# Kernel tuning notes

Hardware: AMD Instinct MI355X
Metric: run time of the kernel (lower is better)

## Reference

```python
import jax, jax.numpy as jnp
import numpy as np
from jax import lax

EMBED_DIM = 384
NUM_GROUPS = 128
GROUP_SIZE = 64
LN_EPS = 1e-5


def setup_inputs() -> dict:
    key = jax.random.key(0)
    k_pts, k1, k2, k3, k4 = jax.random.split(key, 5)
    B, N = 32, 16384
    points = jax.random.normal(k_pts, (B, N, 3), dtype=jnp.float32)
    # local_mlp: Linear(3,128) -> GELU -> Linear(128, embed_dim)
    w1 = jax.random.normal(k1, (3, 128), dtype=jnp.float32) * (1.0 / np.sqrt(3))
    b1 = jax.random.normal(k2, (128,), dtype=jnp.float32) * 0.01
    w2 = jax.random.normal(k3, (128, EMBED_DIM), dtype=jnp.float32) * (1.0 / np.sqrt(128))
    b2 = jax.random.normal(k4, (EMBED_DIM,), dtype=jnp.float32) * 0.01
    ln_scale = jnp.ones((EMBED_DIM,), dtype=jnp.float32)
    ln_bias = jnp.zeros((EMBED_DIM,), dtype=jnp.float32)
    return {"points": points, "w1": w1, "b1": b1, "w2": w2, "b2": b2,
            "ln_scale": ln_scale, "ln_bias": ln_bias}


def _farthest_point_sample(points, num_samples):
    # points: [B, N, 3]. Deterministic start at index 0 (torch uses randint).
    B, N, _ = points.shape

    def step(carry, _):
        distance, farthest = carry  # [B, N], [B]
        centroid = jnp.take_along_axis(points, farthest[:, None, None], axis=1)  # [B,1,3]
        d = jnp.sum((points - centroid) ** 2, axis=-1)  # [B, N]
        distance = jnp.minimum(distance, d)
        nxt = jnp.argmax(distance, axis=-1).astype(jnp.int32)
        return (distance, nxt), farthest

    init = (jnp.full((B, N), jnp.inf, dtype=points.dtype),
            jnp.zeros((B,), dtype=jnp.int32))
    _, idx = lax.scan(step, init, None, length=num_samples)  # [S, B]
    return idx.T  # [B, S]


def reference(points, w1, b1, w2, b2, ln_scale, ln_bias):
    B, N, _ = points.shape
    centroid_idx = _farthest_point_sample(points, NUM_GROUPS)  # [B, G]
    centroids = jnp.take_along_axis(
        points, centroid_idx[:, :, None].astype(jnp.int32), axis=1)  # [B, G, 3]

    # squared distances (same ordering as torch.cdist for topk); matmul form
    # avoids materializing a [B, G, N, 3] diff tensor.
    c2 = jnp.sum(centroids ** 2, axis=-1)  # [B, G]
    p2 = jnp.sum(points ** 2, axis=-1)     # [B, N]
    dist2 = c2[:, :, None] + p2[:, None, :] - 2.0 * jnp.einsum(
        'bgc,bnc->bgn', centroids, points)  # [B, G, N]

    # k smallest -> top_k of negated distances
    _, neighbor_idx = lax.top_k(-dist2, GROUP_SIZE)  # [B, G, K]

    batch_ix = jnp.arange(B)[:, None, None]
    grouped = points[batch_ix, neighbor_idx]  # [B, G, K, 3]
    local_coords = grouped - centroids[:, :, None, :]  # [B, G, K, 3]

    h = jax.nn.gelu(local_coords @ w1 + b1, approximate=False)  # [B,G,K,128]
    feats = h @ w2 + b2  # [B, G, K, D]
    tokens = jnp.mean(feats, axis=2)  # [B, G, D]

    mu = jnp.mean(tokens, axis=-1, keepdims=True)
    var = jnp.mean((tokens - mu) ** 2, axis=-1, keepdims=True)
    tokens_ln = (tokens - mu) * lax.rsqrt(var + LN_EPS) * ln_scale + ln_bias
    return centroids, tokens_ln
```

## Files before the change

### kernel.cpp

```cpp
#include <hip/hip_runtime.h>
#include <math.h>

#define BB 32
#define NN 16384
#define GG 128
#define KK 64
#define HH 128
#define DD 384
#define LN_EPS 1e-5f
#define NBUCK 2048
#define CANDCAP 1024

__device__ __forceinline__ float sq3(float x, float y, float z) {
    return __fadd_rn(__fadd_rn(__fmul_rn(x, x), __fmul_rn(y, y)), __fmul_rn(z, z));
}

__global__ void prep_kernel(const float* __restrict__ w2, float* __restrict__ w2t) {
    int i = blockIdx.x * 256 + threadIdx.x;
    if (i < HH * DD) {
        int f = i >> 7;
        int k = i & 127;
        w2t[i] = w2[k * DD + f];
    }
}

__global__ __launch_bounds__(512) void fps_kernel(const float* __restrict__ pts,
                                                  float* __restrict__ cent_out,
                                                  float4* __restrict__ cent_pad) {
    const int b = blockIdx.x;
    const int tid = threadIdx.x;
    const float* p = pts + (size_t)b * NN * 3;

    float x[32], y[32], z[32], dist[32];
#pragma unroll
    for (int j = 0; j < 32; j++) {
        int n = j * 512 + tid;
        x[j] = p[n * 3 + 0];
        y[j] = p[n * 3 + 1];
        z[j] = p[n * 3 + 2];
        dist[j] = INFINITY;
    }

    __shared__ float cenx, ceny, cenz;
    __shared__ float wv[8];
    __shared__ int wi[8];

    if (tid == 0) { cenx = p[0]; ceny = p[1]; cenz = p[2]; }
    __syncthreads();

    for (int it = 0; it < GG; it++) {
        float cx = cenx, cy = ceny, cz = cenz;
        if (tid == 0) {
            float* co = cent_out + ((size_t)b * GG + it) * 3;
            co[0] = cx; co[1] = cy; co[2] = cz;
            cent_pad[b * GG + it] = make_float4(cx, cy, cz, sq3(cx, cy, cz));
        }
        float bv0 = -INFINITY, bv1 = -INFINITY, bv2 = -INFINITY, bv3 = -INFINITY;
        int bi0 = 0, bi1 = 0, bi2 = 0, bi3 = 0;
#pragma unroll
        for (int j = 0; j < 32; j++) {
            float dx = __fsub_rn(x[j], cx);
            float dy = __fsub_rn(y[j], cy);
            float dz = __fsub_rn(z[j], cz);
            float d = sq3(dx, dy, dz);
            float dj = fminf(dist[j], d);
            dist[j] = dj;
            int n = j * 512 + tid;
            switch (j & 3) {
                case 0: if (dj > bv0) { bv0 = dj; bi0 = n; } break;
                case 1: if (dj > bv1) { bv1 = dj; bi1 = n; } break;
                case 2: if (dj > bv2) { bv2 = dj; bi2 = n; } break;
                case 3: if (dj > bv3) { bv3 = dj; bi3 = n; } break;
            }
        }
        float fv = bv0; int fi = bi0;
        if (bv1 > fv || (bv1 == fv && bi1 < fi)) { fv = bv1; fi = bi1; }
        if (bv2 > fv || (bv2 == fv && bi2 < fi)) { fv = bv2; fi = bi2; }
        if (bv3 > fv || (bv3 == fv && bi3 < fi)) { fv = bv3; fi = bi3; }
#pragma unroll
        for (int off = 32; off >= 1; off >>= 1) {
            float ov = __shfl_down(fv, off);
            int oi = __shfl_down(fi, off);
            if (ov > fv || (ov == fv && oi < fi)) { fv = ov; fi = oi; }
        }
        int lane = tid & 63, wid = tid >> 6;
        if (lane == 0) { wv[wid] = fv; wi[wid] = fi; }
        __syncthreads();
        if (tid == 0) {
            float gv = wv[0]; int gi = wi[0];
            for (int w = 1; w < 8; w++) {
                if (wv[w] > gv || (wv[w] == gv && wi[w] < gi)) { gv = wv[w]; gi = wi[w]; }
            }
            const float* wp = p + (size_t)gi * 3;
            cenx = wp[0]; ceny = wp[1]; cenz = wp[2];
        }
        __syncthreads();
    }
}

__global__ __launch_bounds__(256) void group_kernel(
    const float* __restrict__ pts, const float4* __restrict__ cent_pad,
    const float* __restrict__ w1, const float* __restrict__ b1,
    const float* __restrict__ w2t, const float* __restrict__ b2,
    const float* __restrict__ lns, const float* __restrict__ lnb,
    float* __restrict__ tok_out) {
    __shared__ __align__(16) unsigned hist[NBUCK];
    __shared__ unsigned long long cand[CANDCAP];
    __shared__ int selIdx[KK];
    __shared__ float4 localPt[KK];
    __shared__ float w1s[3 * HH];
    __shared__ float b1s[HH];
    __shared__ __align__(16) float hbar[HH];
    __shared__ float partial[256];
    __shared__ float red2[8];
    __shared__ float toks[DD];
    __shared__ int waveSum[4];
    __shared__ unsigned long long wmin[4];
    __shared__ unsigned TA_S;
    __shared__ int cntS;
    __shared__ unsigned long long lastS;
    __shared__ float muS, rstdS;

    const int tid = threadIdx.x;
    int bid = blockIdx.x;
    int xcd = bid & 7, sub = bid >> 3;
    int b = xcd * 4 + (sub >> 7);
    int g = sub & 127;

    const float* p = pts + (size_t)b * NN * 3;
    float4 c4 = cent_pad[b * GG + g];

    for (int i = tid; i < 3 * HH; i += 256) w1s[i] = w1[i];
    if (tid < HH) b1s[tid] = b1[tid];
    for (int i = tid; i < NBUCK; i += 256) hist[i] = 0;
    if (tid == 0) cntS = 0;
    __syncthreads();

    unsigned key[64];
#pragma unroll
    for (int i = 0; i < 64; i++) {
        int n = i * 256 + tid;
        float px = p[n * 3], py = p[n * 3 + 1], pz = p[n * 3 + 2];
        float p2 = sq3(px, py, pz);
        float dot = __fadd_rn(__fadd_rn(__fmul_rn(c4.x, px), __fmul_rn(c4.y, py)),
                              __fmul_rn(c4.z, pz));
        float d = __fsub_rn(__fadd_rn(c4.w, p2), __fmul_rn(2.0f, dot));
        unsigned u = __float_as_uint(d);
        u ^= (u & 0x80000000u) ? 0xFFFFFFFFu : 0x80000000u;
        key[i] = u;
        atomicAdd(&hist[u >> 21], 1u);
    }
    __syncthreads();

    {
        uint4 h0 = ((const uint4*)hist)[tid * 2];
        uint4 h1 = ((const uint4*)hist)[tid * 2 + 1];
        int loc[8] = {(int)h0.x, (int)h0.y, (int)h0.z, (int)h0.w,
                      (int)h1.x, (int)h1.y, (int)h1.z, (int)h1.w};
        int s = 0;
#pragma unroll
        for (int j = 0; j < 8; j++) s += loc[j];
        int lane = tid & 63, wid = tid >> 6;
        int v = s;
#pragma unroll
        for (int off = 1; off < 64; off <<= 1) {
            int o = __shfl_up(v, off);
            if (lane >= off) v += o;
        }
        if (lane == 63) waveSum[wid] = v;
        __syncthreads();
        int base = 0;
        for (int w = 0; w < wid; w++) base += waveSum[w];
        int c = base + v - s;
#pragma unroll
        for (int j = 0; j < 8; j++) {
            if (c < KK && c + loc[j] >= KK) TA_S = (unsigned)(tid * 8 + j);
            c += loc[j];
        }
        __syncthreads();
    }
    unsigned TA = TA_S;

#pragma unroll
    for (int i = 0; i < 64; i++) {
        unsigned u = key[i];
        if ((u >> 21) <= TA) {
            int pos = atomicAdd(&cntS, 1);
            if (pos < CANDCAP)
                cand[pos] = ((unsigned long long)u << 32) | (unsigned)(i * 256 + tid);
        }
    }
    __syncthreads();
    int cnt = cntS;

    if (cnt <= CANDCAP) {
        for (int c0 = tid; c0 < cnt; c0 += 256) {
            unsigned long long pr = cand[c0];
            int rank = 0;
            for (int j = 0; j < cnt; j++) rank += (cand[j] < pr);
            if (rank < KK) selIdx[rank] = (int)(unsigned)pr;
        }
        __syncthreads();
    } else {
        if (tid == 0) lastS = 0ull;
        __syncthreads();
        for (int r = 0; r < KK; r++) {
            unsigned long long last = lastS;
            unsigned long long best = 0xFFFFFFFFFFFFFFFFull;
#pragma unroll
            for (int i = 0; i < 64; i++) {
                unsigned long long pr =
                    ((unsigned long long)key[i] << 32) | (unsigned)(i * 256 + tid);
                if ((r == 0 || pr > last) && pr < best) best = pr;
            }
            unsigned blo = (unsigned)best, bhi = (unsigned)(best >> 32);
#pragma unroll
            for (int off = 32; off >= 1; off >>= 1) {
                unsigned olo = __shfl_down(blo, off);
                unsigned ohi = __shfl_down(bhi, off);
                unsigned long long ob = ((unsigned long long)ohi << 32) | olo;
                unsigned long long cur = ((unsigned long long)bhi << 32) | blo;
                if (ob < cur) { blo = olo; bhi = ohi; }
            }
            int lane = tid & 63, wid = tid >> 6;
            if (lane == 0) wmin[wid] = ((unsigned long long)bhi << 32) | blo;
            __syncthreads();
            if (tid == 0) {
                unsigned long long m = wmin[0];
                for (int w = 1; w < 4; w++) if (wmin[w] < m) m = wmin[w];
                selIdx[r] = (int)(unsigned)m;
                lastS = m;
            }
            __syncthreads();
        }
    }

    if (tid < KK) {
        int n = selIdx[tid];
        float px = p[n * 3], py = p[n * 3 + 1], pz = p[n * 3 + 2];
        localPt[tid] = make_float4(px - c4.x, py - c4.y, pz - c4.z, 0.f);
    }
    __syncthreads();
    {
        int f = tid & 127, half = tid >> 7;
        float wa = w1s[f], wb = w1s[HH + f], wc = w1s[2 * HH + f], bb = b1s[f];
        float s = 0.f;
        for (int k = half * 32; k < half * 32 + 32; k++) {
            float4 lp = localPt[k];
            float a = lp.x * wa + lp.y * wb + lp.z * wc + bb;
            float hh = 0.5f * a * (1.0f + erff(a * 0.70710678118654752440f));
            s += hh;
        }
        partial[tid] = s;
    }
    __syncthreads();
    if (tid < HH) hbar[tid] = (partial[tid] + partial[tid + HH]) * (1.0f / 64.0f);
    __syncthreads();
    for (int f2 = tid; f2 < DD; f2 += 256) {
        const float4* wrow = (const float4*)(w2t + f2 * HH);
        const float4* hb = (const float4*)hbar;
        float acc = b2[f2];
#pragma unroll 8
        for (int q = 0; q < 32; q++) {
            float4 w4 = wrow[q];
            float4 h4 = hb[q];
            acc += h4.x * w4.x + h4.y * w4.y + h4.z * w4.z + h4.w * w4.w;
        }
        toks[f2] = acc;
    }
    __syncthreads();
    {
        float s1 = 0.f, s2 = 0.f;
        for (int f2 = tid; f2 < DD; f2 += 256) {
            float v = toks[f2];
            s1 += v;
            s2 += v * v;
        }
#pragma unroll
        for (int off = 32; off >= 1; off >>= 1) {
            s1 += __shfl_down(s1, off);
            s2 += __shfl_down(s2, off);
        }
        int lane = tid & 63, wid = tid >> 6;
        if (lane == 0) { partial[wid] = s1; red2[wid] = s2; }
        __syncthreads();
        if (tid == 0) {
            float t1 = partial[0] + partial[1] + partial[2] + partial[3];
            float t2 = red2[0] + red2[1] + red2[2] + red2[3];
            float mu = t1 / (float)DD;
            float var = t2 / (float)DD - mu * mu;
            muS = mu;
            rstdS = rsqrtf(var + LN_EPS);
        }
        __syncthreads();
    }
    float mu = muS, rstd = rstdS;
    float* outp = tok_out + ((size_t)b * GG + g) * DD;
    for (int f2 = tid; f2 < DD; f2 += 256) {
        outp[f2] = (toks[f2] - mu) * rstd * lns[f2] + lnb[f2];
    }
}

extern "C" void kernel_launch(void* const* d_in, const int* in_sizes, int n_in,
                              void* d_out, int out_size, void* d_ws, size_t ws_size,
                              hipStream_t stream) {
    const float* pts = (const float*)d_in[0];
    const float* w1 = (const float*)d_in[1];
    const float* b1 = (const float*)d_in[2];
    const float* w2 = (const float*)d_in[3];
    const float* b2 = (const float*)d_in[4];
    const float* lns = (const float*)d_in[5];
    const float* lnb = (const float*)d_in[6];
    float* out = (float*)d_out;

    float4* cent_pad = (float4*)d_ws;
    float* w2t = (float*)((char*)d_ws + BB * GG * sizeof(float4));

    prep_kernel<<<192, 256, 0, stream>>>(w2, w2t);
    fps_kernel<<<BB, 512, 0, stream>>>(pts, out, cent_pad);
    group_kernel<<<BB * GG, 256, 0, stream>>>(pts, cent_pad, w1, b1, w2t, b2, lns, lnb,
                                              out + BB * GG * 3);
}
```

Baseline: 629.9 us.

## Split FPS across four blocks per batch and use wave-per-group kNN selection

```diff
diff --git a/kernel.cpp b/kernel.cpp
--- a/kernel.cpp
+++ b/kernel.cpp
@@ -8,296 +8,299 @@
 #define HH 128
 #define DD 384
 #define LN_EPS 1e-5f
-#define NBUCK 2048
-#define CANDCAP 1024
+#define CAP 1024
+#define FPSB 4
+#define FPSP (NN / FPSB)
 
 __device__ __forceinline__ float sq3(float x, float y, float z) {
     return __fadd_rn(__fadd_rn(__fmul_rn(x, x), __fmul_rn(y, y)), __fmul_rn(z, z));
 }
 
-__global__ void prep_kernel(const float* __restrict__ w2, float* __restrict__ w2t) {
+__device__ __forceinline__ unsigned distkey(float px, float py, float pz, float4 c4) {
+    float p2 = sq3(px, py, pz);
+    float dot = __fadd_rn(__fadd_rn(__fmul_rn(c4.x, px), __fmul_rn(c4.y, py)),
+                          __fmul_rn(c4.z, pz));
+    float d = __fsub_rn(__fadd_rn(c4.w, p2), __fmul_rn(2.0f, dot));
+    unsigned u = __float_as_uint(d);
+    return u ^ ((u & 0x80000000u) ? 0xFFFFFFFFu : 0x80000000u);
+}
+
+__device__ __forceinline__ unsigned lanerank(unsigned long long m) {
+    unsigned r = __builtin_amdgcn_mbcnt_lo((unsigned)m, 0);
+    return __builtin_amdgcn_mbcnt_hi((unsigned)(m >> 32), r);
+}
+
+__global__ void prep_kernel(const float* __restrict__ w2, float* __restrict__ w2t,
+                            unsigned* __restrict__ zeroArea) {
     int i = blockIdx.x * 256 + threadIdx.x;
     if (i < HH * DD) {
-        int f = i >> 7;
-        int k = i & 127;
+        int f = i >> 7, k = i & 127;
         w2t[i] = w2[k * DD + f];
     }
-}
-
-__global__ __launch_bounds__(512) void fps_kernel(const float* __restrict__ pts,
-                                                  float* __restrict__ cent_out,
-                                                  float4* __restrict__ cent_pad) {
-    const int b = blockIdx.x;
-    const int tid = threadIdx.x;
-    const float* p = pts + (size_t)b * NN * 3;
-
-    float x[32], y[32], z[32], dist[32];
-#pragma unroll
-    for (int j = 0; j < 32; j++) {
-        int n = j * 512 + tid;
-        x[j] = p[n * 3 + 0];
-        y[j] = p[n * 3 + 1];
-        z[j] = p[n * 3 + 2];
-        dist[j] = INFINITY;
-    }
-
-    __shared__ float cenx, ceny, cenz;
+    int j = i - HH * DD;
+    if (j >= 0 && j < 12288) zeroArea[j] = 0u;
+}
+
+__global__ __launch_bounds__(512, 2) void fps_kernel(
+    const float* __restrict__ pts, float* __restrict__ cent_out,
+    float4* __restrict__ cent_pad, unsigned long long* __restrict__ gslot,
+    unsigned* __restrict__ garr) {
+    __shared__ float xs[FPSP], ys[FPSP], zs[FPSP], ds[FPSP];
     __shared__ float wv[8];
     __shared__ int wi[8];
-
-    if (tid == 0) { cenx = p[0]; ceny = p[1]; cenz = p[2]; }
+    __shared__ float cen[2][3];
+    const int tid = threadIdx.x;
+    const int x = blockIdx.x & 7, j = blockIdx.x >> 3;
+    const int b = x * 4 + (j >> 2), quarter = j & 3;
+    const float* pb = pts + (size_t)b * NN * 3;
+    const int start = quarter * FPSP;
+    const float4* p4s = (const float4*)(pb + start * 3);
+
+    for (int t = tid; t < FPSP / 4; t += 512) {
+        float4 A = p4s[3 * t], Bv = p4s[3 * t + 1], Cv = p4s[3 * t + 2];
+        ((float4*)xs)[t] = make_float4(A.x, A.w, Bv.z, Cv.y);
+        ((float4*)ys)[t] = make_float4(A.y, Bv.x, Bv.w, Cv.z);
+        ((float4*)zs)[t] = make_float4(A.z, Bv.y, Cv.x, Cv.w);
+        ((float4*)ds)[t] = make_float4(INFINITY, INFINITY, INFINITY, INFINITY);
+    }
     __syncthreads();
 
+    float cx = pb[0], cy = pb[1], cz = pb[2];
+
     for (int it = 0; it < GG; it++) {
-        float cx = cenx, cy = ceny, cz = cenz;
-        if (tid == 0) {
+        if (quarter == 0 && tid == 0) {
             float* co = cent_out + ((size_t)b * GG + it) * 3;
             co[0] = cx; co[1] = cy; co[2] = cz;
             cent_pad[b * GG + it] = make_float4(cx, cy, cz, sq3(cx, cy, cz));
         }
-        float bv0 = -INFINITY, bv1 = -INFINITY, bv2 = -INFINITY, bv3 = -INFINITY;
-        int bi0 = 0, bi1 = 0, bi2 = 0, bi3 = 0;
-#pragma unroll
-        for (int j = 0; j < 32; j++) {
-            float dx = __fsub_rn(x[j], cx);
-            float dy = __fsub_rn(y[j], cy);
-            float dz = __fsub_rn(z[j], cz);
-            float d = sq3(dx, dy, dz);
-            float dj = fminf(dist[j], d);
-            dist[j] = dj;
-            int n = j * 512 + tid;
-            switch (j & 3) {
-                case 0: if (dj > bv0) { bv0 = dj; bi0 = n; } break;
-                case 1: if (dj > bv1) { bv1 = dj; bi1 = n; } break;
-                case 2: if (dj > bv2) { bv2 = dj; bi2 = n; } break;
-                case 3: if (dj > bv3) { bv3 = dj; bi3 = n; } break;
-            }
-        }
-        float fv = bv0; int fi = bi0;
-        if (bv1 > fv || (bv1 == fv && bi1 < fi)) { fv = bv1; fi = bi1; }
-        if (bv2 > fv || (bv2 == fv && bi2 < fi)) { fv = bv2; fi = bi2; }
-        if (bv3 > fv || (bv3 == fv && bi3 < fi)) { fv = bv3; fi = bi3; }
+        if (it == GG - 1) break;
+
+        float fv = -INFINITY;
+        int fi = 0;
+#pragma unroll
+        for (int s = 0; s < 8; s++) {
+            int n = s * 512 + tid;
+            float dx = __fsub_rn(xs[n], cx);
+            float dy = __fsub_rn(ys[n], cy);
+            float dz = __fsub_rn(zs[n], cz);
+            float dd = sq3(dx, dy, dz);
+            float od = ds[n];
+            float dj = fminf(od, dd);
+            if (dd < od) ds[n] = dd;
+            if (dj > fv) { fv = dj; fi = start + n; }
+        }
 #pragma unroll
         for (int off = 32; off >= 1; off >>= 1) {
             float ov = __shfl_down(fv, off);
             int oi = __shfl_down(fi, off);
             if (ov > fv || (ov == fv && oi < fi)) { fv = ov; fi = oi; }
         }
-        int lane = tid & 63, wid = tid >> 6;
-        if (lane == 0) { wv[wid] = fv; wi[wid] = fi; }
+        if ((tid & 63) == 0) { wv[tid >> 6] = fv; wi[tid >> 6] = fi; }
         __syncthreads();
+        const int slotI = b * GG + it;
         if (tid == 0) {
-            float gv = wv[0]; int gi = wi[0];
-            for (int w = 1; w < 8; w++) {
+            float gv = wv[0];
+            int gi = wi[0];
+            for (int w = 1; w < 8; w++)
                 if (wv[w] > gv || (wv[w] == gv && wi[w] < gi)) { gv = wv[w]; gi = wi[w]; }
-            }
-            const float* wp = p + (size_t)gi * 3;
-            cenx = wp[0]; ceny = wp[1]; cenz = wp[2];
+            unsigned long long packed =
+                ((unsigned long long)__float_as_uint(gv) << 32) |
+                (unsigned)(0xFFFFFFFFu - (unsigned)gi);
+            atomicMax(&gslot[slotI], packed);
+            __hip_atomic_fetch_add(&garr[slotI], 1u, __ATOMIC_RELEASE,
+                                   __HIP_MEMORY_SCOPE_AGENT);
+            while (__hip_atomic_load(&garr[slotI], __ATOMIC_ACQUIRE,
+                                     __HIP_MEMORY_SCOPE_AGENT) < (unsigned)FPSB)
+                __builtin_amdgcn_s_sleep(1);
+            unsigned long long w = __hip_atomic_load(&gslot[slotI], __ATOMIC_RELAXED,
+                                                     __HIP_MEMORY_SCOPE_AGENT);
+            int idx = (int)(0xFFFFFFFFu - (unsigned)w);
+            const float* wp = pb + (size_t)idx * 3;
+            cen[it & 1][0] = wp[0]; cen[it & 1][1] = wp[1]; cen[it & 1][2] = wp[2];
         }
         __syncthreads();
-    }
-}
-
-__global__ __launch_bounds__(256) void group_kernel(
+        cx = cen[it & 1][0]; cy = cen[it & 1][1]; cz = cen[it & 1][2];
+    }
+}
+
+__global__ __launch_bounds__(256, 4) void group_kernel(
     const float* __restrict__ pts, const float4* __restrict__ cent_pad,
     const float* __restrict__ w1, const float* __restrict__ b1,
     const float* __restrict__ w2t, const float* __restrict__ b2,
     const float* __restrict__ lns, const float* __restrict__ lnb,
     float* __restrict__ tok_out) {
-    __shared__ __align__(16) unsigned hist[NBUCK];
-    __shared__ unsigned long long cand[CANDCAP];
-    __shared__ int selIdx[KK];
-    __shared__ float4 localPt[KK];
-    __shared__ float w1s[3 * HH];
-    __shared__ float b1s[HH];
-    __shared__ __align__(16) float hbar[HH];
-    __shared__ float partial[256];
-    __shared__ float red2[8];
-    __shared__ float toks[DD];
-    __shared__ int waveSum[4];
-    __shared__ unsigned long long wmin[4];
-    __shared__ unsigned TA_S;
-    __shared__ int cntS;
-    __shared__ unsigned long long lastS;
-    __shared__ float muS, rstdS;
-
-    const int tid = threadIdx.x;
-    int bid = blockIdx.x;
-    int xcd = bid & 7, sub = bid >> 3;
-    int b = xcd * 4 + (sub >> 7);
-    int g = sub & 127;
-
+    __shared__ unsigned candKey[4][CAP];
+    __shared__ unsigned short candIdx[4][CAP];
+    __shared__ unsigned short selIdx[4][KK];
+    __shared__ float4 localPt[4][KK];
+    __shared__ __align__(16) float hbar[4][HH];
+
+    const int tid = threadIdx.x, lane = tid & 63, wid = tid >> 6;
+    const int x = blockIdx.x & 7, j = blockIdx.x >> 3;
+    const int b = x * 4 + (j >> 5);
+    const int g = ((j & 31) << 2) + wid;
     const float* p = pts + (size_t)b * NN * 3;
+    const float4* p4 = (const float4*)p;
     float4 c4 = cent_pad[b * GG + g];
 
-    for (int i = tid; i < 3 * HH; i += 256) w1s[i] = w1[i];
-    if (tid < HH) b1s[tid] = b1[tid];
-    for (int i = tid; i < NBUCK; i += 256) hist[i] = 0;
-    if (tid == 0) cntS = 0;
-    __syncthreads();
-
-    unsigned key[64];
-#pragma unroll
-    for (int i = 0; i < 64; i++) {
-        int n = i * 256 + tid;
-        float px = p[n * 3], py = p[n * 3 + 1], pz = p[n * 3 + 2];
-        float p2 = sq3(px, py, pz);
-        float dot = __fadd_rn(__fadd_rn(__fmul_rn(c4.x, px), __fmul_rn(c4.y, py)),
-                              __fmul_rn(c4.z, pz));
-        float d = __fsub_rn(__fadd_rn(c4.w, p2), __fmul_rn(2.0f, dot));
-        unsigned u = __float_as_uint(d);
-        u ^= (u & 0x80000000u) ? 0xFFFFFFFFu : 0x80000000u;
-        key[i] = u;
-        atomicAdd(&hist[u >> 21], 1u);
-    }
-    __syncthreads();
+    unsigned sk[8];
+#pragma unroll
+    for (int s = 0; s < 8; s++) {
+        int n = (s * 64 + lane) * 32;
+        sk[s] = distkey(p[n * 3], p[n * 3 + 1], p[n * 3 + 2], c4);
+    }
+    auto sample_kth = [&](int rank) -> unsigned {
+        unsigned T = 0u;
+        for (int bit = 31; bit >= 0; bit--) {
+            unsigned c = T | (1u << bit);
+            int cnt = 0;
+#pragma unroll
+            for (int s = 0; s < 8; s++) cnt += __popcll(__ballot(sk[s] < c));
+            if (cnt < rank) T = c;
+        }
+        return T;
+    };
+    unsigned* ck = candKey[wid];
+    unsigned short* ci = candIdx[wid];
+    auto collect = [&](unsigned T) -> int {
+        int base = 0;
+        for (int it2 = 0; it2 < 64; it2++) {
+            int q = it2 * 64 + lane;
+            float4 A = p4[3 * q], Bv = p4[3 * q + 1], Cv = p4[3 * q + 2];
+            unsigned kk[4];
+            kk[0] = distkey(A.x, A.y, A.z, c4);
+            kk[1] = distkey(A.w, Bv.x, Bv.y, c4);
+            kk[2] = distkey(Bv.z, Bv.w, Cv.x, c4);
+            kk[3] = distkey(Cv.y, Cv.z, Cv.w, c4);
+#pragma unroll
+            for (int qq = 0; qq < 4; qq++) {
+                bool pred = kk[qq] <= T;
+                unsigned long long m = __ballot(pred);
+                if (pred) {
+                    int pos = base + (int)lanerank(m);
+                    if (pos < CAP) { ck[pos] = kk[qq]; ci[pos] = (unsigned short)(4 * q + qq); }
+                }
+                base += __popcll(m);
+            }
+        }
+        return base;
+    };
+
+    unsigned T1 = sample_kth(16);
+    int c1 = collect(T1);
+    if (c1 > CAP) { T1 = sample_kth(8); c1 = collect(T1); }
+
+    if (c1 >= KK && c1 <= CAP) {
+        unsigned long long pr[16];
+#pragma unroll
+        for (int r = 0; r < 16; r++) {
+            int s = r * 64 + lane;
+            pr[r] = (s < c1) ? ((((unsigned long long)ck[s]) << 16) | ci[s]) : ~0ull;
+        }
+        unsigned long long T = 0ull;
+        for (int bit = 47; bit >= 0; bit--) {
+            unsigned long long c = T | (1ull << bit);
+            int cnt = 0;
+#pragma unroll
+            for (int r = 0; r < 16; r++) cnt += __popcll(__ballot(pr[r] < c));
+            if (cnt < KK) T = c;
+        }
+        int base = 0;
+#pragma unroll
+        for (int r = 0; r < 16; r++) {
+            bool pred = pr[r] <= T;
+            unsigned long long m = __ballot(pred);
+            if (pred) selIdx[wid][base + lanerank(m)] = (unsigned short)(pr[r] & 0xFFFFu);
+            base += __popcll(m);
+        }
+    } else {
+        unsigned long long last = 0ull;
+        for (int r = 0; r < KK; r++) {
+            unsigned long long best = ~0ull;
+            for (int it2 = 0; it2 < 64; it2++) {
+                int q = it2 * 64 + lane;
+                float4 A = p4[3 * q], Bv = p4[3 * q + 1], Cv = p4[3 * q + 2];
+                unsigned kk[4];
+                kk[0] = distkey(A.x, A.y, A.z, c4);
+                kk[1] = distkey(A.w, Bv.x, Bv.y, c4);
+                kk[2] = distkey(Bv.z, Bv.w, Cv.x, c4);
+                kk[3] = distkey(Cv.y, Cv.z, Cv.w, c4);
+#pragma unroll
+                for (int qq = 0; qq < 4; qq++) {
+                    unsigned long long pp =
+                        (((unsigned long long)kk[qq]) << 16) | (unsigned)(4 * q + qq);
+                    if ((r == 0 || pp > last) && pp < best) best = pp;
+                }
+            }
+#pragma unroll
+            for (int off = 32; off >= 1; off >>= 1) {
+                unsigned long long o = __shfl_xor(best, off);
+                if (o < best) best = o;
+            }
+            selIdx[wid][r] = (unsigned short)(best & 0xFFFFu);
+            last = best;
+        }
+    }
 
     {
-        uint4 h0 = ((const uint4*)hist)[tid * 2];
-        uint4 h1 = ((const uint4*)hist)[tid * 2 + 1];
-        int loc[8] = {(int)h0.x, (int)h0.y, (int)h0.z, (int)h0.w,
-                      (int)h1.x, (int)h1.y, (int)h1.z, (int)h1.w};
-        int s = 0;
-#pragma unroll
-        for (int j = 0; j < 8; j++) s += loc[j];
-        int lane = tid & 63, wid = tid >> 6;
-        int v = s;
-#pragma unroll
-        for (int off = 1; off < 64; off <<= 1) {
-            int o = __shfl_up(v, off);
-            if (lane >= off) v += o;
-        }
-        if (lane == 63) waveSum[wid] = v;
-        __syncthreads();
-        int base = 0;
-        for (int w = 0; w < wid; w++) base += waveSum[w];
-        int c = base + v - s;
-#pragma unroll
-        for (int j = 0; j < 8; j++) {
-            if (c < KK && c + loc[j] >= KK) TA_S = (unsigned)(tid * 8 + j);
-            c += loc[j];
-        }
-        __syncthreads();
-    }
-    unsigned TA = TA_S;
-
-#pragma unroll
-    for (int i = 0; i < 64; i++) {
-        unsigned u = key[i];
-        if ((u >> 21) <= TA) {
-            int pos = atomicAdd(&cntS, 1);
-            if (pos < CANDCAP)
-                cand[pos] = ((unsigned long long)u << 32) | (unsigned)(i * 256 + tid);
-        }
-    }
-    __syncthreads();
-    int cnt = cntS;
-
-    if (cnt <= CANDCAP) {
-        for (int c0 = tid; c0 < cnt; c0 += 256) {
-            unsigned long long pr = cand[c0];
-            int rank = 0;
-            for (int j = 0; j < cnt; j++) rank += (cand[j] < pr);
-            if (rank < KK) selIdx[rank] = (int)(unsigned)pr;
-        }
-        __syncthreads();
-    } else {
-        if (tid == 0) lastS = 0ull;
-        __syncthreads();
-        for (int r = 0; r < KK; r++) {
-            unsigned long long last = lastS;
-            unsigned long long best = 0xFFFFFFFFFFFFFFFFull;
-#pragma unroll
-            for (int i = 0; i < 64; i++) {
-                unsigned long long pr =
-                    ((unsigned long long)key[i] << 32) | (unsigned)(i * 256 + tid);
-                if ((r == 0 || pr > last) && pr < best) best = pr;
-            }
-            unsigned blo = (unsigned)best, bhi = (unsigned)(best >> 32);
-#pragma unroll
-            for (int off = 32; off >= 1; off >>= 1) {
-                unsigned olo = __shfl_down(blo, off);
-                unsigned ohi = __shfl_down(bhi, off);
-                unsigned long long ob = ((unsigned long long)ohi << 32) | olo;
-                unsigned long long cur = ((unsigned long long)bhi << 32) | blo;
-                if (ob < cur) { blo = olo; bhi = ohi; }
-            }
-            int lane = tid & 63, wid = tid >> 6;
-            if (lane == 0) wmin[wid] = ((unsigned long long)bhi << 32) | blo;
-            __syncthreads();
-            if (tid == 0) {
-                unsigned long long m = wmin[0];
-                for (int w = 1; w < 4; w++) if (wmin[w] < m) m = wmin[w];
-                selIdx[r] = (int)(unsigned)m;
-                lastS = m;
-            }
-            __syncthreads();
-        }
-    }
-
-    if (tid < KK) {
-        int n = selIdx[tid];
-        float px = p[n * 3], py = p[n * 3 + 1], pz = p[n * 3 + 2];
-        localPt[tid] = make_float4(px - c4.x, py - c4.y, pz - c4.z, 0.f);
-    }
-    __syncthreads();
+        int n = selIdx[wid][lane];
+        localPt[wid][lane] =
+            make_float4(p[n * 3] - c4.x, p[n * 3 + 1] - c4.y, p[n * 3 + 2] - c4.z, 0.f);
+    }
     {
-        int f = tid & 127, half = tid >> 7;
-        float wa = w1s[f], wb = w1s[HH + f], wc = w1s[2 * HH + f], bb = b1s[f];
-        float s = 0.f;
-        for (int k = half * 32; k < half * 32 + 32; k++) {
-            float4 lp = localPt[k];
-            float a = lp.x * wa + lp.y * wb + lp.z * wc + bb;
-            float hh = 0.5f * a * (1.0f + erff(a * 0.70710678118654752440f));
-            s += hh;
-        }
-        partial[tid] = s;
-    }
-    __syncthreads();
-    if (tid < HH) hbar[tid] = (partial[tid] + partial[tid + HH]) * (1.0f / 64.0f);
-    __syncthreads();
-    for (int f2 = tid; f2 < DD; f2 += 256) {
-        const float4* wrow = (const float4*)(w2t + f2 * HH);
-        const float4* hb = (const float4*)hbar;
-        float acc = b2[f2];
-#pragma unroll 8
-        for (int q = 0; q < 32; q++) {
-            float4 w4 = wrow[q];
+        float wa0 = w1[lane], wb0 = w1[HH + lane], wc0 = w1[2 * HH + lane], bb0 = b1[lane];
+        float wa1 = w1[64 + lane], wb1 = w1[HH + 64 + lane], wc1 = w1[2 * HH + 64 + lane],
+              bb1 = b1[64 + lane];
+        float s0 = 0.f, s1 = 0.f;
+        for (int k = 0; k < KK; k++) {
+            float4 lp = localPt[wid][k];
+            float a0 = lp.x * wa0 + lp.y * wb0 + lp.z * wc0 + bb0;
+            float a1 = lp.x * wa1 + lp.y * wb1 + lp.z * wc1 + bb1;
+            s0 += 0.5f * a0 * (1.0f + erff(a0 * 0.70710678118654752440f));
+            s1 += 0.5f * a1 * (1.0f + erff(a1 * 0.70710678118654752440f));
+        }
+        hbar[wid][lane] = s0 * (1.0f / 64.0f);
+        hbar[wid][64 + lane] = s1 * (1.0f / 64.0f);
+    }
+    {
+        const int f0 = lane * 6;
+        float acc0 = b2[f0], acc1 = b2[f0 + 1], acc2 = b2[f0 + 2];
+        float acc3 = b2[f0 + 3], acc4 = b2[f0 + 4], acc5 = b2[f0 + 5];
+        const float4* hb = (const float4*)hbar[wid];
+        for (int q = 0; q < HH / 4; q++) {
             float4 h4 = hb[q];
-            acc += h4.x * w4.x + h4.y * w4.y + h4.z * w4.z + h4.w * w4.w;
-        }
-        toks[f2] = acc;
-    }
-    __syncthreads();
-    {
-        float s1 = 0.f, s2 = 0.f;
-        for (int f2 = tid; f2 < DD; f2 += 256) {
-            float v = toks[f2];
-            s1 += v;
-            s2 += v * v;
-        }
+            const float* w0 = w2t + (size_t)f0 * HH + 4 * q;
+            float4 a = *(const float4*)(w0);
+            float4 bq = *(const float4*)(w0 + HH);
+            float4 cq = *(const float4*)(w0 + 2 * HH);
+            float4 dq = *(const float4*)(w0 + 3 * HH);
+            float4 eq = *(const float4*)(w0 + 4 * HH);
+            float4 fq = *(const float4*)(w0 + 5 * HH);
+            acc0 += h4.x * a.x + h4.y * a.y + h4.z * a.z + h4.w * a.w;
+            acc1 += h4.x * bq.x + h4.y * bq.y + h4.z * bq.z + h4.w * bq.w;
+            acc2 += h4.x * cq.x + h4.y * cq.y + h4.z * cq.z + h4.w * cq.w;
+            acc3 += h4.x * dq.x + h4.y * dq.y + h4.z * dq.z + h4.w * dq.w;
+            acc4 += h4.x * eq.x + h4.y * eq.y + h4.z * eq.z + h4.w * eq.w;
+            acc5 += h4.x * fq.x + h4.y * fq.y + h4.z * fq.z + h4.w * fq.w;
+        }
+        float s1v = acc0 + acc1 + acc2 + acc3 + acc4 + acc5;
+        float s2v = acc0 * acc0 + acc1 * acc1 + acc2 * acc2 + acc3 * acc3 +
+                    acc4 * acc4 + acc5 * acc5;
 #pragma unroll
         for (int off = 32; off >= 1; off >>= 1) {
-            s1 += __shfl_down(s1, off);
-            s2 += __shfl_down(s2, off);
-        }
-        int lane = tid & 63, wid = tid >> 6;
-        if (lane == 0) { partial[wid] = s1; red2[wid] = s2; }
-        __syncthreads();
-        if (tid == 0) {
-            float t1 = partial[0] + partial[1] + partial[2] + partial[3];
-            float t2 = red2[0] + red2[1] + red2[2] + red2[3];
-            float mu = t1 / (float)DD;
-            float var = t2 / (float)DD - mu * mu;
-            muS = mu;
-            rstdS = rsqrtf(var + LN_EPS);
-        }
-        __syncthreads();
-    }
-    float mu = muS, rstd = rstdS;
-    float* outp = tok_out + ((size_t)b * GG + g) * DD;
-    for (int f2 = tid; f2 < DD; f2 += 256) {
-        outp[f2] = (toks[f2] - mu) * rstd * lns[f2] + lnb[f2];
+            s1v += __shfl_xor(s1v, off);
+            s2v += __shfl_xor(s2v, off);
+        }
+        float mu = s1v / (float)DD;
+        float var = s2v / (float)DD - mu * mu;
+        float rstd = rsqrtf(var + LN_EPS);
+        float* outp = tok_out + ((size_t)b * GG + g) * DD + f0;
+        outp[0] = (acc0 - mu) * rstd * lns[f0] + lnb[f0];
+        outp[1] = (acc1 - mu) * rstd * lns[f0 + 1] + lnb[f0 + 1];
+        outp[2] = (acc2 - mu) * rstd * lns[f0 + 2] + lnb[f0 + 2];
+        outp[3] = (acc3 - mu) * rstd * lns[f0 + 3] + lnb[f0 + 3];
+        outp[4] = (acc4 - mu) * rstd * lns[f0 + 4] + lnb[f0 + 4];
+        outp[5] = (acc5 - mu) * rstd * lns[f0 + 5] + lnb[f0 + 5];
     }
 }
 
@@ -314,10 +317,12 @@
     float* out = (float*)d_out;
 
     float4* cent_pad = (float4*)d_ws;
-    float* w2t = (float*)((char*)d_ws + BB * GG * sizeof(float4));
-
-    prep_kernel<<<192, 256, 0, stream>>>(w2, w2t);
-    fps_kernel<<<BB, 512, 0, stream>>>(pts, out, cent_pad);
-    group_kernel<<<BB * GG, 256, 0, stream>>>(pts, cent_pad, w1, b1, w2t, b2, lns, lnb,
-                                              out + BB * GG * 3);
-}
+    float* w2t = (float*)((char*)d_ws + 65536);
+    unsigned long long* gslot = (unsigned long long*)((char*)d_ws + 262144);
+    unsigned* garr = (unsigned*)((char*)d_ws + 294912);
+
+    prep_kernel<<<256, 256, 0, stream>>>(w2, w2t, (unsigned*)gslot);
+    fps_kernel<<<128, 512, 0, stream>>>(pts, out, cent_pad, gslot, garr);
+    group_kernel<<<1024, 256, 0, stream>>>(pts, cent_pad, w1, b1, w2t, b2, lns, lnb,
+                                           out + BB * GG * 3);
+}
```

After: 780.8 us. +24.0%, slower.
